# Performance work log

Measured on AMD Instinct MI355X. Metric: run time of the kernel, lower is better.

Reference implementation:

```python
import jax, jax.numpy as jnp
import numpy as np

WH, WW = 8, 8            # window size
N = WH * WW              # tokens per window = 64
DIM = 512
HEADS = 16
NW = 64                  # windows per image (mask batch)
B = 1024                 # total windows = 16 images * 64 windows
CPB_HIDDEN = 512


def _make_buffers():
    # relative coords table for CPB-MLP: [1, 2*WH-1, 2*WW-1, 2]
    rch = np.arange(-(WH - 1), WH, dtype=np.float32)
    rcw = np.arange(-(WW - 1), WW, dtype=np.float32)
    table = np.stack(np.meshgrid(rch, rcw, indexing='ij'), axis=-1)[None]
    table[..., 0] /= (WH - 1)
    table[..., 1] /= (WW - 1)
    table *= 8.0
    table = np.sign(table) * np.log2(np.abs(table) + 1.0) / 3.0
    # relative position index: [N, N]
    coords = np.stack(np.meshgrid(np.arange(WH), np.arange(WW), indexing='ij'), 0).reshape(2, -1)
    rel = coords[:, :, None] - coords[:, None, :]      # [2, N, N]
    rel = rel.transpose(1, 2, 0).astype(np.int64)
    rel[..., 0] += WH - 1
    rel[..., 1] += WW - 1
    rel[..., 0] *= 2 * WW - 1
    idx = rel.sum(-1)
    return jnp.asarray(table, jnp.float32), jnp.asarray(idx, jnp.int32)


def setup_inputs() -> dict:
    key = jax.random.key(0)
    ks = jax.random.split(key, 8)
    table, idx = _make_buffers()
    return {
        'x': jax.random.normal(ks[0], (B, N, DIM), jnp.float32),
        'mask': jax.random.normal(ks[1], (NW, N, N), jnp.float32),
        'qkv_w': jax.random.normal(ks[2], (3 * DIM, DIM), jnp.float32) * 0.02,
        'q_bias': jnp.zeros((DIM,), jnp.float32),
        'v_bias': jnp.zeros((DIM,), jnp.float32),
        'logit_scale': jnp.full((HEADS, 1, 1), np.log(10.0), jnp.float32),
        'cpb_w1': jax.random.normal(ks[3], (CPB_HIDDEN, 2), jnp.float32) * 0.02,
        'cpb_b1': jnp.zeros((CPB_HIDDEN,), jnp.float32),
        'cpb_w2': jax.random.normal(ks[4], (HEADS, CPB_HIDDEN), jnp.float32) * 0.02,
        'proj_w': jax.random.normal(ks[5], (DIM, DIM), jnp.float32) * 0.02,
        'proj_b': jnp.zeros((DIM,), jnp.float32),
        'rel_coords_table': table,
        'rel_pos_index': idx,
    }


def _l2norm(t):
    n = jnp.sqrt(jnp.sum(t * t, axis=-1, keepdims=True))
    return t / jnp.maximum(n, 1e-12)


def reference(x, mask, qkv_w, q_bias, v_bias, logit_scale, cpb_w1, cpb_b1,
              cpb_w2, proj_w, proj_b, rel_coords_table, rel_pos_index):
    Bq, Nq, C = x.shape
    qkv_b = jnp.concatenate([q_bias, jnp.zeros_like(v_bias), v_bias])
    qkv = x @ qkv_w.T + qkv_b                                  # [B, N, 3C]
    qkv = qkv.reshape(Bq, Nq, 3, HEADS, C // HEADS).transpose(2, 0, 3, 1, 4)
    q, k, v = qkv[0], qkv[1], qkv[2]                           # [B, H, N, D]
    attn = jnp.einsum('bhnd,bhmd->bhnm', _l2norm(q), _l2norm(k))
    scale = jnp.exp(jnp.minimum(logit_scale, jnp.log(jnp.float32(100.0))))
    attn = attn * scale                                        # [B, H, N, N]
    # CPB-MLP relative position bias
    hidden = jax.nn.relu(rel_coords_table @ cpb_w1.T + cpb_b1)  # [1, 2WH-1, 2WW-1, 512]
    bias_table = (hidden @ cpb_w2.T).reshape(-1, HEADS)         # [(2WH-1)(2WW-1), H]
    rel_bias = bias_table[rel_pos_index.reshape(-1)].reshape(Nq, Nq, HEADS)
    rel_bias = 16.0 * jax.nn.sigmoid(rel_bias.transpose(2, 0, 1))  # [H, N, N]
    attn = attn + rel_bias[None]
    nW = mask.shape[0]
    attn = attn.reshape(Bq // nW, nW, HEADS, Nq, Nq) + mask[None, :, None]
    attn = jax.nn.softmax(attn.reshape(Bq, HEADS, Nq, Nq), axis=-1)
    out = jnp.einsum('bhnm,bhmd->bhnd', attn, v)
    out = out.transpose(0, 2, 1, 3).reshape(Bq, Nq, C)
    return out @ proj_w.T + proj_b
```

## Files before the change

kernel.cpp:

```cpp
#include <hip/hip_runtime.h>
#include <hip/hip_bf16.h>

typedef __bf16 bf16;
typedef __bf16 bf16x4 __attribute__((ext_vector_type(4)));
typedef __bf16 bf16x8 __attribute__((ext_vector_type(8)));
typedef float floatx4 __attribute__((ext_vector_type(4)));

#define MFMA16(a, b, c) __builtin_amdgcn_mfma_f32_16x16x32_bf16((a), (b), (c), 0, 0, 0)

static constexpr long OFF_QKV   = 0;
static constexpr long OFF_XB    = 201326592;
static constexpr long OFF_WQKV  = 268435456;
static constexpr long OFF_WPROJ = 270008320;
static constexpr long OFF_BT    = 270532608;
static constexpr long OFF_RB    = 270548992;

__device__ __forceinline__ void load_lds16(const bf16* g, bf16* l) {
  __builtin_amdgcn_global_load_lds((const __attribute__((address_space(1))) void*)(g),
                                   (__attribute__((address_space(3))) void*)(l), 16, 0, 0);
}

__global__ __launch_bounds__(256) void cvt_f32_bf16(const float* __restrict__ src,
                                                    bf16* __restrict__ dst, int n8) {
  int i = blockIdx.x * 256 + threadIdx.x;
  if (i < n8) {
    const float4* s = (const float4*)src;
    float4 a = s[2 * i], b = s[2 * i + 1];
    bf16x8 o;
    o[0] = (bf16)a.x; o[1] = (bf16)a.y; o[2] = (bf16)a.z; o[3] = (bf16)a.w;
    o[4] = (bf16)b.x; o[5] = (bf16)b.y; o[6] = (bf16)b.z; o[7] = (bf16)b.w;
    ((bf16x8*)dst)[i] = o;
  }
}

__global__ __launch_bounds__(256) void cpb_mlp(const float* __restrict__ table,
                                               const float* __restrict__ w1,
                                               const float* __restrict__ b1,
                                               const float* __restrict__ w2,
                                               float* __restrict__ bias_table) {
  __shared__ float hid[512];
  const int e = blockIdx.x;
  const float t0 = table[e * 2 + 0], t1 = table[e * 2 + 1];
  for (int j = threadIdx.x; j < 512; j += 256) {
    float hv = t0 * w1[j * 2 + 0] + t1 * w1[j * 2 + 1] + b1[j];
    hid[j] = hv > 0.f ? hv : 0.f;
  }
  __syncthreads();
  const int hd = threadIdx.x >> 4, l = threadIdx.x & 15;
  float p = 0.f;
  for (int j = l; j < 512; j += 16) p += hid[j] * w2[hd * 512 + j];
  #pragma unroll
  for (int d = 8; d >= 1; d >>= 1) p += __shfl_xor(p, d, 16);
  if (l == 0) bias_table[e * 16 + hd] = p;
}

__global__ __launch_bounds__(256) void cpb_gather(const float* __restrict__ bias_table,
                                                  const int* __restrict__ idx,
                                                  float* __restrict__ rel_bias) {
  int f = blockIdx.x * 256 + threadIdx.x;
  int h = f >> 12, ij = f & 4095;
  float v = bias_table[idx[ij] * 16 + h];
  rel_bias[f] = 16.f / (1.f + __expf(-v));
}

template <int NN, bool QKV>
__global__ __launch_bounds__(512, 2) void gemm_bt(const bf16* __restrict__ A,
                                                  const bf16* __restrict__ Bt,
                                                  void* __restrict__ outv,
                                                  const float* __restrict__ bias_a,
                                                  const float* __restrict__ bias_b) {
  constexpr int K = 512;
  constexpr int KT = K / 64;
  constexpr int nblk = NN / 128;
  __shared__ alignas(16) bf16 As[3][256 * 64];
  __shared__ alignas(16) bf16 Bs[3][128 * 64];
  const int tid = threadIdx.x;
  const int lane = tid & 63;
  const int wv = tid >> 6;
  const int bid = blockIdx.x;
  const int xcd = bid & 7;
  const int g = bid >> 3;
  const int mb = xcd * 32 + (g & 31);
  const int nb = g >> 5;
  const long m0 = (long)mb * 256;
  const int n0 = nb * 128;
  const int wm = (wv & 3) * 64;
  const int wn = (wv >> 2) * 64;
  const int cl = lane & 15;
  const int cq = lane >> 4;

  const floatx4 fzero = {0.f, 0.f, 0.f, 0.f};
  floatx4 acc[4][4];
  #pragma unroll
  for (int i = 0; i < 4; ++i)
    #pragma unroll
    for (int j = 0; j < 4; ++j) acc[i][j] = fzero;

  int srow[4], sc8[4];
  #pragma unroll
  for (int r = 0; r < 4; ++r) {
    int s = r * 512 + tid;
    srow[r] = s >> 3;
    sc8[r] = (s & 7) ^ (srow[r] & 7);
  }
  const int wbase = tid & ~63;

  auto stage = [&](int buf, int kt) {
    const int k0 = kt * 64;
    #pragma unroll
    for (int r = 0; r < 4; ++r) {
      const bf16* ga = A + (m0 + srow[r]) * (long)K + (k0 + sc8[r] * 8);
      load_lds16(ga, &As[buf][(r * 512 + wbase) * 8]);
    }
    #pragma unroll
    for (int r = 0; r < 2; ++r) {
      const bf16* gb = Bt + (long)(n0 + srow[r]) * K + (k0 + sc8[r] * 8);
      load_lds16(gb, &Bs[buf][(r * 512 + wbase) * 8]);
    }
  };

  auto compute = [&](int buf) {
    #pragma unroll
    for (int kk = 0; kk < 2; ++kk) {
      bf16x8 af[4], bfr[4];
      const int gg = kk * 4 + cq;
      #pragma unroll
      for (int t = 0; t < 4; ++t) {
        const int mr = wm + t * 16 + cl;
        af[t] = *(const bf16x8*)&As[buf][(mr * 8 + (gg ^ (mr & 7))) * 8];
        const int nr = wn + t * 16 + cl;
        bfr[t] = *(const bf16x8*)&Bs[buf][(nr * 8 + (gg ^ (nr & 7))) * 8];
      }
      __builtin_amdgcn_s_setprio(1);
      #pragma unroll
      for (int i = 0; i < 4; ++i)
        #pragma unroll
        for (int j = 0; j < 4; ++j)
          acc[i][j] = MFMA16(bfr[j], af[i], acc[i][j]);
      __builtin_amdgcn_s_setprio(0);
    }
  };

  stage(0, 0);
  stage(1, 1);
  asm volatile("s_waitcnt vmcnt(6)" ::: "memory");
  __builtin_amdgcn_s_barrier();

  #pragma unroll
  for (int kt = 0; kt < KT; ++kt) {
    if (kt + 2 < KT) stage((kt + 2) % 3, kt + 2);
    __builtin_amdgcn_sched_barrier(0);
    compute(kt % 3);
    __builtin_amdgcn_sched_barrier(0);
    if (kt + 2 < KT)
      asm volatile("s_waitcnt vmcnt(6)" ::: "memory");
    else if (kt + 1 < KT)
      asm volatile("s_waitcnt vmcnt(0)" ::: "memory");
    if (kt + 1 < KT) __builtin_amdgcn_s_barrier();
  }

  const int cq4 = cq * 4;
  #pragma unroll
  for (int i = 0; i < 4; ++i) {
    const long m = m0 + wm + i * 16 + cl;
    #pragma unroll
    for (int j = 0; j < 4; ++j) {
      const int nbase = n0 + wn + j * 16 + cq4;
      if constexpr (QKV) {
        float4 bb = {0.f, 0.f, 0.f, 0.f};
        if (nbase < 512) bb = *(const float4*)&bias_a[nbase];
        else if (nbase >= 1024) bb = *(const float4*)&bias_b[nbase - 1024];
        bf16x4 o;
        o[0] = (bf16)(acc[i][j][0] + bb.x);
        o[1] = (bf16)(acc[i][j][1] + bb.y);
        o[2] = (bf16)(acc[i][j][2] + bb.z);
        o[3] = (bf16)(acc[i][j][3] + bb.w);
        *(bf16x4*)((bf16*)outv + m * NN + nbase) = o;
      } else {
        const float4 bb = *(const float4*)&bias_a[nbase];
        float4 o;
        o.x = acc[i][j][0] + bb.x;
        o.y = acc[i][j][1] + bb.y;
        o.z = acc[i][j][2] + bb.z;
        o.w = acc[i][j][3] + bb.w;
        *(float4*)((float*)outv + m * NN + nbase) = o;
      }
    }
  }
}

__global__ __launch_bounds__(256, 5) void attn_kernel(const bf16* __restrict__ qkv,
                                                      const float* __restrict__ mask,
                                                      const float* __restrict__ lscale,
                                                      const float* __restrict__ rel_bias,
                                                      bf16* __restrict__ out) {
  const int bid = blockIdx.x;
  const int xcd = bid & 7;
  const int t = bid >> 3;
  const int p = xcd + ((t >> 1) << 3);
  const int b = p >> 3;
  const int h = ((p & 7) << 1) | (t & 1);
  const int wi = b & 63;
  const int tid = threadIdx.x;
  const int lane = tid & 63;
  const int wv = tid >> 6;
  const int cl = lane & 15;
  const int cq = lane >> 4;

  __shared__ alignas(16) bf16 smem[12544];
  bf16* qh_s = smem;
  bf16* ql_s = smem + 2560;
  bf16* kh_s = smem + 5120;
  bf16* kl_s = smem + 7680;
  bf16* vT   = smem + 10240;
  bf16* ps   = smem;

  {
    const int r = tid >> 2, seg = tid & 3;
    const bf16* base = qkv + (long)(b * 64 + r) * 1536 + h * 32 + seg * 8;
    float f[8], ss;
    bf16x8 hi, lo;

    bf16x8 qv = *(const bf16x8*)(base);
    ss = 0.f;
    #pragma unroll
    for (int j = 0; j < 8; ++j) { f[j] = (float)qv[j]; ss += f[j] * f[j]; }
    ss += __shfl_xor(ss, 1, 4); ss += __shfl_xor(ss, 2, 4);
    float s1 = 1.f / fmaxf(sqrtf(ss), 1e-12f);
    #pragma unroll
    for (int j = 0; j < 8; ++j) {
      float xn = f[j] * s1;
      bf16 xh = (bf16)xn;
      hi[j] = xh; lo[j] = (bf16)(xn - (float)xh);
    }
    *(bf16x8*)&qh_s[r * 40 + seg * 8] = hi;
    *(bf16x8*)&ql_s[r * 40 + seg * 8] = lo;

    bf16x8 kv = *(const bf16x8*)(base + 512);
    ss = 0.f;
    #pragma unroll
    for (int j = 0; j < 8; ++j) { f[j] = (float)kv[j]; ss += f[j] * f[j]; }
    ss += __shfl_xor(ss, 1, 4); ss += __shfl_xor(ss, 2, 4);
    s1 = 1.f / fmaxf(sqrtf(ss), 1e-12f);
    #pragma unroll
    for (int j = 0; j < 8; ++j) {
      float xn = f[j] * s1;
      bf16 xh = (bf16)xn;
      hi[j] = xh; lo[j] = (bf16)(xn - (float)xh);
    }
    *(bf16x8*)&kh_s[r * 40 + seg * 8] = hi;
    *(bf16x8*)&kl_s[r * 40 + seg * 8] = lo;

    bf16x8 vv = *(const bf16x8*)(base + 1024);
    #pragma unroll
    for (int j = 0; j < 8; ++j) vT[(seg * 8 + j) * 72 + r] = vv[j];
  }
  __syncthreads();

  const float sc = __expf(fminf(lscale[h], 4.6051701859880914f));

  const int mrow = wv * 16 + cl;
  const bf16x8 aqh = *(const bf16x8*)&qh_s[mrow * 40 + cq * 8];
  const bf16x8 aql = *(const bf16x8*)&ql_s[mrow * 40 + cq * 8];
  floatx4 sacc[4];
  #pragma unroll
  for (int nt = 0; nt < 4; ++nt) {
    const int nr = nt * 16 + cl;
    const bf16x8 bkh = *(const bf16x8*)&kh_s[nr * 40 + cq * 8];
    const bf16x8 bkl = *(const bf16x8*)&kl_s[nr * 40 + cq * 8];
    floatx4 a = {0.f, 0.f, 0.f, 0.f};
    a = MFMA16(aql, bkh, a);
    a = MFMA16(aqh, bkl, a);
    a = MFMA16(aqh, bkh, a);
    sacc[nt] = a;
  }
  __syncthreads();

  float pw[4][4];
  #pragma unroll
  for (int rg = 0; rg < 4; ++rg) {
    const int row = wv * 16 + cq * 4 + rg;
    const float* rbp = rel_bias + h * 4096 + row * 64;
    const float* mkp = mask + wi * 4096 + row * 64;
    float mxv = -1e30f;
    #pragma unroll
    for (int nt = 0; nt < 4; ++nt) {
      float s = sacc[nt][rg] * sc + rbp[nt * 16 + cl] + mkp[nt * 16 + cl];
      pw[rg][nt] = s;
      mxv = fmaxf(mxv, s);
    }
    #pragma unroll
    for (int d = 8; d >= 1; d >>= 1) mxv = fmaxf(mxv, __shfl_xor(mxv, d, 16));
    float sm = 0.f;
    #pragma unroll
    for (int nt = 0; nt < 4; ++nt) {
      float e = __expf(pw[rg][nt] - mxv);
      pw[rg][nt] = e;
      sm += e;
    }
    #pragma unroll
    for (int d = 8; d >= 1; d >>= 1) sm += __shfl_xor(sm, d, 16);
    const float inv = 1.f / sm;
    #pragma unroll
    for (int nt = 0; nt < 4; ++nt)
      ps[row * 72 + nt * 16 + cl] = (bf16)(pw[rg][nt] * inv);
  }

  floatx4 oacc[2];
  oacc[0] = (floatx4){0.f, 0.f, 0.f, 0.f};
  oacc[1] = (floatx4){0.f, 0.f, 0.f, 0.f};
  #pragma unroll
  for (int ks = 0; ks < 2; ++ks) {
    const bf16x8 ap = *(const bf16x8*)&ps[(wv * 16 + cl) * 72 + ks * 32 + cq * 8];
    #pragma unroll
    for (int nt = 0; nt < 2; ++nt) {
      const bf16x8 bv = *(const bf16x8*)&vT[(nt * 16 + cl) * 72 + ks * 32 + cq * 8];
      oacc[nt] = MFMA16(bv, ap, oacc[nt]);
    }
  }
  const long obase = (long)(b * 64 + wv * 16 + cl) * 512 + h * 32 + cq * 4;
  #pragma unroll
  for (int nt = 0; nt < 2; ++nt) {
    bf16x4 o;
    #pragma unroll
    for (int r = 0; r < 4; ++r) o[r] = (bf16)oacc[nt][r];
    *(bf16x4*)&out[obase + nt * 16] = o;
  }
}

extern "C" void kernel_launch(void* const* d_in, const int* in_sizes, int n_in,
                              void* d_out, int out_size, void* d_ws, size_t ws_size,
                              hipStream_t stream) {
  const float* x      = (const float*)d_in[0];
  const float* mask   = (const float*)d_in[1];
  const float* qkv_w  = (const float*)d_in[2];
  const float* q_bias = (const float*)d_in[3];
  const float* v_bias = (const float*)d_in[4];
  const float* lsc    = (const float*)d_in[5];
  const float* cpb_w1 = (const float*)d_in[6];
  const float* cpb_b1 = (const float*)d_in[7];
  const float* cpb_w2 = (const float*)d_in[8];
  const float* proj_w = (const float*)d_in[9];
  const float* proj_b = (const float*)d_in[10];
  const float* table  = (const float*)d_in[11];
  const int*   relidx = (const int*)d_in[12];

  char* ws = (char*)d_ws;
  bf16* qkvb   = (bf16*)(ws + OFF_QKV);
  bf16* xb     = (bf16*)(ws + OFF_XB);
  bf16* wqkv   = (bf16*)(ws + OFF_WQKV);
  bf16* wproj  = (bf16*)(ws + OFF_WPROJ);
  float* btab  = (float*)(ws + OFF_BT);
  float* rbias = (float*)(ws + OFF_RB);

  cvt_f32_bf16<<<16384, 256, 0, stream>>>(x, xb, 65536 * 512 / 8);
  cvt_f32_bf16<<<384, 256, 0, stream>>>(qkv_w, wqkv, 1536 * 512 / 8);
  cvt_f32_bf16<<<128, 256, 0, stream>>>(proj_w, wproj, 512 * 512 / 8);
  cpb_mlp<<<225, 256, 0, stream>>>(table, cpb_w1, cpb_b1, cpb_w2, btab);
  cpb_gather<<<256, 256, 0, stream>>>(btab, relidx, rbias);

  gemm_bt<1536, true><<<256 * 12, 512, 0, stream>>>(xb, wqkv, (void*)qkvb, q_bias, v_bias);
  attn_kernel<<<16384, 256, 0, stream>>>(qkvb, mask, lsc, rbias, xb);
  gemm_bt<512, false><<<256 * 4, 512, 0, stream>>>(xb, wproj, d_out, proj_b, nullptr);
}
```

Baseline: 608.7 us.

## Enlarge GEMM tile to 256x256 with 4-stage k=32 pipeline

The shared bf16 GEMM moves from 256x128 tiles to 256x256 tiles. Each wave now computes a 128x64 sub-tile (8x4 accumulators). The K loop becomes 16 half-steps of k=32 using a 4-deep LDS ring with a new XOR swizzle, and the B-tile staging is split across two barrier phases so loads overlap MFMA work. The goal is higher arithmetic intensity, less global/LDS traffic per FLOP and fewer blocks. The cost is more registers, which may hurt occupancy at launch_bounds(512,2), and fewer blocks (1536/512) to fill the CUs.

```diff
diff --git a/kernel.cpp b/kernel.cpp
--- a/kernel.cpp
+++ b/kernel.cpp
@@ -70,98 +70,115 @@
                                                   const float* __restrict__ bias_a,
                                                   const float* __restrict__ bias_b) {
   constexpr int K = 512;
-  constexpr int KT = K / 64;
-  constexpr int nblk = NN / 128;
-  __shared__ alignas(16) bf16 As[3][256 * 64];
-  __shared__ alignas(16) bf16 Bs[3][128 * 64];
+  constexpr int nblk = NN / 256;
+  __shared__ alignas(16) bf16 As[4][8192];
+  __shared__ alignas(16) bf16 Bs[4][8192];
   const int tid = threadIdx.x;
   const int lane = tid & 63;
   const int wv = tid >> 6;
   const int bid = blockIdx.x;
   const int xcd = bid & 7;
   const int g = bid >> 3;
-  const int mb = xcd * 32 + (g & 31);
-  const int nb = g >> 5;
+  const int mb = xcd * 32 + g / nblk;
+  const int nb = g % nblk;
   const long m0 = (long)mb * 256;
-  const int n0 = nb * 128;
-  const int wm = (wv & 3) * 64;
-  const int wn = (wv >> 2) * 64;
+  const int n0 = nb * 256;
+  const int wm = (wv >> 2) * 128;
+  const int wn = (wv & 3) * 64;
   const int cl = lane & 15;
   const int cq = lane >> 4;
+  const int wbase = tid & ~63;
+  const int sx = (cq ^ ((cl >> 1) & 3)) << 3;
 
   const floatx4 fzero = {0.f, 0.f, 0.f, 0.f};
-  floatx4 acc[4][4];
-  #pragma unroll
-  for (int i = 0; i < 4; ++i)
+  floatx4 acc[8][4];
+  #pragma unroll
+  for (int i = 0; i < 8; ++i)
     #pragma unroll
     for (int j = 0; j < 4; ++j) acc[i][j] = fzero;
 
-  int srow[4], sc8[4];
-  #pragma unroll
-  for (int r = 0; r < 4; ++r) {
-    int s = r * 512 + tid;
-    srow[r] = s >> 3;
-    sc8[r] = (s & 7) ^ (srow[r] & 7);
-  }
-  const int wbase = tid & ~63;
-
-  auto stage = [&](int buf, int kt) {
-    const int k0 = kt * 64;
-    #pragma unroll
-    for (int r = 0; r < 4; ++r) {
-      const bf16* ga = A + (m0 + srow[r]) * (long)K + (k0 + sc8[r] * 8);
-      load_lds16(ga, &As[buf][(r * 512 + wbase) * 8]);
-    }
-    #pragma unroll
-    for (int r = 0; r < 2; ++r) {
-      const bf16* gb = Bt + (long)(n0 + srow[r]) * K + (k0 + sc8[r] * 8);
-      load_lds16(gb, &Bs[buf][(r * 512 + wbase) * 8]);
+  auto stageA = [&](int kh) {
+    #pragma unroll
+    for (int o = 0; o < 2; ++o) {
+      const int s = o * 512 + tid;
+      const int r = s >> 2;
+      const int gl = (s & 3) ^ ((s >> 3) & 3);
+      const bf16* ga = A + (m0 + r) * (long)K + kh * 32 + gl * 8;
+      load_lds16(ga, &As[kh & 3][(o * 512 + wbase) * 8]);
     }
   };
-
-  auto compute = [&](int buf) {
-    #pragma unroll
-    for (int kk = 0; kk < 2; ++kk) {
-      bf16x8 af[4], bfr[4];
-      const int gg = kk * 4 + cq;
-      #pragma unroll
-      for (int t = 0; t < 4; ++t) {
-        const int mr = wm + t * 16 + cl;
-        af[t] = *(const bf16x8*)&As[buf][(mr * 8 + (gg ^ (mr & 7))) * 8];
-        const int nr = wn + t * 16 + cl;
-        bfr[t] = *(const bf16x8*)&Bs[buf][(nr * 8 + (gg ^ (nr & 7))) * 8];
-      }
-      __builtin_amdgcn_s_setprio(1);
-      #pragma unroll
-      for (int i = 0; i < 4; ++i)
-        #pragma unroll
-        for (int j = 0; j < 4; ++j)
-          acc[i][j] = MFMA16(bfr[j], af[i], acc[i][j]);
-      __builtin_amdgcn_s_setprio(0);
+  auto stageB = [&](int kh) {
+    #pragma unroll
+    for (int o = 0; o < 2; ++o) {
+      const int s = o * 512 + tid;
+      const int r = s >> 2;
+      const int gl = (s & 3) ^ ((s >> 3) & 3);
+      const bf16* gb = Bt + (long)(n0 + r) * K + kh * 32 + gl * 8;
+      load_lds16(gb, &Bs[kh & 3][(o * 512 + wbase) * 8]);
     }
   };
-
-  stage(0, 0);
-  stage(1, 1);
-  asm volatile("s_waitcnt vmcnt(6)" ::: "memory");
+  auto waitvm = [&](int n) {
+    if (n == 8) asm volatile("s_waitcnt vmcnt(8)" ::: "memory");
+    else if (n == 4) asm volatile("s_waitcnt vmcnt(4)" ::: "memory");
+    else if (n == 0) asm volatile("s_waitcnt vmcnt(0)" ::: "memory");
+  };
+
+  auto kstep = [&](int h, int slot, bool doStage, int vmN, bool lastH) {
+    bf16x8 af[8];
+    if (doStage) stageA(h + 3);
+    #pragma unroll
+    for (int m = 0; m < 8; ++m) {
+      const int r = wm + m * 16 + cl;
+      af[m] = *(const bf16x8*)&As[slot][r * 32 + sx];
+    }
+    bf16x8 b0[2];
+    #pragma unroll
+    for (int n = 0; n < 2; ++n) {
+      const int r = wn + n * 16 + cl;
+      b0[n] = *(const bf16x8*)&Bs[slot][r * 32 + sx];
+    }
+    __builtin_amdgcn_s_setprio(1);
+    #pragma unroll
+    for (int i = 0; i < 8; ++i) {
+      acc[i][0] = MFMA16(b0[0], af[i], acc[i][0]);
+      acc[i][1] = MFMA16(b0[1], af[i], acc[i][1]);
+    }
+    __builtin_amdgcn_s_setprio(0);
+    __builtin_amdgcn_sched_barrier(0);
+    __builtin_amdgcn_s_barrier();
+    if (doStage) stageB(h + 3);
+    bf16x8 b1[2];
+    #pragma unroll
+    for (int n = 0; n < 2; ++n) {
+      const int r = wn + (2 + n) * 16 + cl;
+      b1[n] = *(const bf16x8*)&Bs[slot][r * 32 + sx];
+    }
+    __builtin_amdgcn_s_setprio(1);
+    #pragma unroll
+    for (int i = 0; i < 8; ++i) {
+      acc[i][2] = MFMA16(b1[0], af[i], acc[i][2]);
+      acc[i][3] = MFMA16(b1[1], af[i], acc[i][3]);
+    }
+    __builtin_amdgcn_s_setprio(0);
+    __builtin_amdgcn_sched_barrier(0);
+    waitvm(vmN);
+    if (!lastH) __builtin_amdgcn_s_barrier();
+  };
+
+  stageA(0); stageB(0); stageA(1); stageB(1); stageA(2); stageB(2);
+  asm volatile("s_waitcnt vmcnt(8)" ::: "memory");
   __builtin_amdgcn_s_barrier();
 
-  #pragma unroll
-  for (int kt = 0; kt < KT; ++kt) {
-    if (kt + 2 < KT) stage((kt + 2) % 3, kt + 2);
-    __builtin_amdgcn_sched_barrier(0);
-    compute(kt % 3);
-    __builtin_amdgcn_sched_barrier(0);
-    if (kt + 2 < KT)
-      asm volatile("s_waitcnt vmcnt(6)" ::: "memory");
-    else if (kt + 1 < KT)
-      asm volatile("s_waitcnt vmcnt(0)" ::: "memory");
-    if (kt + 1 < KT) __builtin_amdgcn_s_barrier();
-  }
+  #pragma unroll 4
+  for (int h = 0; h < 12; ++h) kstep(h, h & 3, true, 8, false);
+  kstep(12, 0, true, 8, false);
+  kstep(13, 1, false, 4, false);
+  kstep(14, 2, false, 0, false);
+  kstep(15, 3, false, -1, true);
 
   const int cq4 = cq * 4;
   #pragma unroll
-  for (int i = 0; i < 4; ++i) {
+  for (int i = 0; i < 8; ++i) {
     const long m = m0 + wm + i * 16 + cl;
     #pragma unroll
     for (int j = 0; j < 4; ++j) {
@@ -359,7 +376,7 @@
   cpb_mlp<<<225, 256, 0, stream>>>(table, cpb_w1, cpb_b1, cpb_w2, btab);
   cpb_gather<<<256, 256, 0, stream>>>(btab, relidx, rbias);
 
-  gemm_bt<1536, true><<<256 * 12, 512, 0, stream>>>(xb, wqkv, (void*)qkvb, q_bias, v_bias);
+  gemm_bt<1536, true><<<1536, 512, 0, stream>>>(xb, wqkv, (void*)qkvb, q_bias, v_bias);
   attn_kernel<<<16384, 256, 0, stream>>>(qkvb, mask, lsc, rbias, xb);
-  gemm_bt<512, false><<<256 * 4, 512, 0, stream>>>(xb, wproj, d_out, proj_b, nullptr);
-}
+  gemm_bt<512, false><<<512, 512, 0, stream>>>(xb, wproj, d_out, proj_b, nullptr);
+}
```

Result: faster. 540.7 us (-11.2%).
